# Performance work log

Measured on AMD Instinct MI355X. Metric: run time of the kernel, lower is better.

Reference implementation:

```python
import jax, jax.numpy as jnp
import numpy as np

B, L, D = 8, 4096, 768
EPS = 1e-5


def layer_norm(x, g, b):
    mu = jnp.mean(x, axis=-1, keepdims=True)
    var = jnp.mean(jnp.square(x - mu), axis=-1, keepdims=True)
    return (x - mu) * jax.lax.rsqrt(var + EPS) * g + b


def conv1d_same(x_blc, w_oik, b_o):
    # x_blc: [B, L, C] -> torch Conv1d(C, C, 3, padding=1) on [B, C, L]
    x_ncw = jnp.swapaxes(x_blc, 1, 2)
    y = jax.lax.conv_general_dilated(
        x_ncw, w_oik, window_strides=(1,), padding=[(1, 1)],
        dimension_numbers=("NCW", "OIW", "NCW"))
    y = y + b_o[None, :, None]
    return jnp.swapaxes(y, 1, 2)


def simple_ssm(u, a_p, b_p, c_p, d_p):
    # Diagonal SSM: h_t = sigmoid(a)*h_{t-1} + b*u_t ; y_t = c*h_t + d*u_t
    a = jax.nn.sigmoid(a_p)  # [D]

    def step(h, ut):  # h, ut: [B, D]
        h = a * h + b_p * ut
        return h, c_p * h

    h0 = jnp.zeros((u.shape[0], u.shape[2]), u.dtype)
    _, y = jax.lax.scan(step, h0, jnp.swapaxes(u, 0, 1))  # y: [L, B, D]
    return jnp.swapaxes(y, 0, 1) + d_p * u


def setup_inputs() -> dict:
    key = jax.random.key(0)
    ks = jax.random.split(key, 16)
    s_lin = 1.0 / np.sqrt(D)
    s_conv = 1.0 / np.sqrt(3 * D)
    return {
        "x": jax.random.normal(ks[0], (B, L, D), jnp.float32),
        "ln_g": jnp.ones((D,), jnp.float32),
        "ln_b": jnp.zeros((D,), jnp.float32),
        "Wi": jax.random.normal(ks[1], (D, 2 * D), jnp.float32) * s_lin,
        "bi": jnp.zeros((2 * D,), jnp.float32),
        "Wf_conv": jax.random.normal(ks[2], (D, D, 3), jnp.float32) * s_conv,
        "bf_conv": jnp.zeros((D,), jnp.float32),
        "af": jax.random.normal(ks[3], (D,), jnp.float32),
        "bf": jax.random.normal(ks[4], (D,), jnp.float32) * 0.5,
        "cf": jax.random.normal(ks[5], (D,), jnp.float32) * 0.5,
        "df": jax.random.normal(ks[6], (D,), jnp.float32) * 0.5,
        "Wb_conv": jax.random.normal(ks[7], (D, D, 3), jnp.float32) * s_conv,
        "bb_conv": jnp.zeros((D,), jnp.float32),
        "ab": jax.random.normal(ks[8], (D,), jnp.float32),
        "bb": jax.random.normal(ks[9], (D,), jnp.float32) * 0.5,
        "cb": jax.random.normal(ks[10], (D,), jnp.float32) * 0.5,
        "db": jax.random.normal(ks[11], (D,), jnp.float32) * 0.5,
        "Wo": jax.random.normal(ks[12], (D, D), jnp.float32) * s_lin,
        "bo": jnp.zeros((D,), jnp.float32),
    }


def reference(x, ln_g, ln_b, Wi, bi, Wf_conv, bf_conv, af, bf, cf, df,
              Wb_conv, bb_conv, ab, bb, cb, db, Wo, bo):
    residual = x
    xn = layer_norm(x, ln_g, ln_b)
    proj = xn @ Wi + bi                      # [B, L, 2D]
    xg, z = proj[..., :D], proj[..., D:]
    # forward branch
    f = conv1d_same(xg, Wf_conv, bf_conv)
    f = simple_ssm(f, af, bf, cf, df)
    # backward branch (flip along sequence)
    b_in = jnp.flip(xg, axis=1)
    bb_out = conv1d_same(b_in, Wb_conv, bb_conv)
    bb_out = simple_ssm(bb_out, ab, bb, cb, db)
    bb_out = jnp.flip(bb_out, axis=1)
    zg = jax.nn.silu(z)
    y = f * zg + bb_out * zg
    return y @ Wo + bo + residual
```

## Files before the change

kernel.cpp:

```cpp
#include <hip/hip_runtime.h>
#include <cstdint>
#include <cstddef>
#include <math.h>

#define L_SEQ 4096
#define D_DIM 768
#define B_SZ 8
#define M_ROWS (B_SZ * L_SEQ)
#define CHUNK 64

typedef __bf16 bf16x8 __attribute__((ext_vector_type(8)));
typedef float floatx4 __attribute__((ext_vector_type(4)));

#define GLP(p)  ((__attribute__((address_space(1))) const void*)(const void*)(p))
#define LDSP(p) ((__attribute__((address_space(3))) void*)(void*)(p))

__global__ __launch_bounds__(256) void ln_kernel(const float* __restrict__ x,
                                                 const float* __restrict__ g,
                                                 const float* __restrict__ b,
                                                 __bf16* __restrict__ xn) {
  __shared__ float red[256];
  const int tid = threadIdx.x;
  const size_t row = blockIdx.x;
  const float* xr = x + row * D_DIM;
  float v0 = xr[tid];
  float v1 = xr[tid + 256];
  float v2 = xr[tid + 512];
  red[tid] = v0 + v1 + v2;
  __syncthreads();
  for (int off = 128; off > 0; off >>= 1) {
    if (tid < off) red[tid] += red[tid + off];
    __syncthreads();
  }
  float mu = red[0] * (1.0f / D_DIM);
  __syncthreads();
  float d0 = v0 - mu, d1 = v1 - mu, d2 = v2 - mu;
  red[tid] = d0 * d0 + d1 * d1 + d2 * d2;
  __syncthreads();
  for (int off = 128; off > 0; off >>= 1) {
    if (tid < off) red[tid] += red[tid + off];
    __syncthreads();
  }
  float rs = rsqrtf(red[0] * (1.0f / D_DIM) + 1e-5f);
  __bf16* xo = xn + row * D_DIM;
  xo[tid]       = (__bf16)(d0 * rs * g[tid]       + b[tid]);
  xo[tid + 256] = (__bf16)(d1 * rs * g[tid + 256] + b[tid + 256]);
  xo[tid + 512] = (__bf16)(d2 * rs * g[tid + 512] + b[tid + 512]);
}


#define VMW(n) asm volatile("s_waitcnt vmcnt(" #n ")" ::: "memory")
#define BARR   asm volatile("s_barrier" ::: "memory")
#define MF(a, b, c) __builtin_amdgcn_mfma_f32_16x16x32_bf16((a), (b), (c), 0, 0, 0)
#define LDV(off) (*(const bf16x8*)(smem + (off)))

#define RDA(BUF, MOFF) do { \
  aR0k0 = LDV((BUF)*65536 + aoff + (MOFF) + ck0);        aR0k1 = LDV((BUF)*65536 + aoff + (MOFF) + ck1); \
  aR1k0 = LDV((BUF)*65536 + aoff + (MOFF) + 2048 + ck0); aR1k1 = LDV((BUF)*65536 + aoff + (MOFF) + 2048 + ck1); \
  aR2k0 = LDV((BUF)*65536 + aoff + (MOFF) + 4096 + ck0); aR2k1 = LDV((BUF)*65536 + aoff + (MOFF) + 4096 + ck1); \
  aR3k0 = LDV((BUF)*65536 + aoff + (MOFF) + 6144 + ck0); aR3k1 = LDV((BUF)*65536 + aoff + (MOFF) + 6144 + ck1); \
} while (0)

#define RDB01(BUF) do { \
  bN0k0 = LDV((BUF)*65536 + boff + ck0);        bN0k1 = LDV((BUF)*65536 + boff + ck1); \
  bN1k0 = LDV((BUF)*65536 + boff + 2048 + ck0); bN1k1 = LDV((BUF)*65536 + boff + 2048 + ck1); \
} while (0)

#define RDB23(BUF) do { \
  bN2k0 = LDV((BUF)*65536 + boff + 4096 + ck0); bN2k1 = LDV((BUF)*65536 + boff + 4096 + ck1); \
  bN3k0 = LDV((BUF)*65536 + boff + 6144 + ck0); bN3k1 = LDV((BUF)*65536 + boff + 6144 + ck1); \
} while (0)

#define MMQ01(AI) do { \
  acc[(AI)+0][0] = MF(aR0k0, bN0k0, acc[(AI)+0][0]); acc[(AI)+0][0] = MF(aR0k1, bN0k1, acc[(AI)+0][0]); \
  acc[(AI)+0][1] = MF(aR0k0, bN1k0, acc[(AI)+0][1]); acc[(AI)+0][1] = MF(aR0k1, bN1k1, acc[(AI)+0][1]); \
  acc[(AI)+1][0] = MF(aR1k0, bN0k0, acc[(AI)+1][0]); acc[(AI)+1][0] = MF(aR1k1, bN0k1, acc[(AI)+1][0]); \
  acc[(AI)+1][1] = MF(aR1k0, bN1k0, acc[(AI)+1][1]); acc[(AI)+1][1] = MF(aR1k1, bN1k1, acc[(AI)+1][1]); \
  acc[(AI)+2][0] = MF(aR2k0, bN0k0, acc[(AI)+2][0]); acc[(AI)+2][0] = MF(aR2k1, bN0k1, acc[(AI)+2][0]); \
  acc[(AI)+2][1] = MF(aR2k0, bN1k0, acc[(AI)+2][1]); acc[(AI)+2][1] = MF(aR2k1, bN1k1, acc[(AI)+2][1]); \
  acc[(AI)+3][0] = MF(aR3k0, bN0k0, acc[(AI)+3][0]); acc[(AI)+3][0] = MF(aR3k1, bN0k1, acc[(AI)+3][0]); \
  acc[(AI)+3][1] = MF(aR3k0, bN1k0, acc[(AI)+3][1]); acc[(AI)+3][1] = MF(aR3k1, bN1k1, acc[(AI)+3][1]); \
} while (0)

#define MMQ23(AI) do { \
  acc[(AI)+0][2] = MF(aR0k0, bN2k0, acc[(AI)+0][2]); acc[(AI)+0][2] = MF(aR0k1, bN2k1, acc[(AI)+0][2]); \
  acc[(AI)+0][3] = MF(aR0k0, bN3k0, acc[(AI)+0][3]); acc[(AI)+0][3] = MF(aR0k1, bN3k1, acc[(AI)+0][3]); \
  acc[(AI)+1][2] = MF(aR1k0, bN2k0, acc[(AI)+1][2]); acc[(AI)+1][2] = MF(aR1k1, bN2k1, acc[(AI)+1][2]); \
  acc[(AI)+1][3] = MF(aR1k0, bN3k0, acc[(AI)+1][3]); acc[(AI)+1][3] = MF(aR1k1, bN3k1, acc[(AI)+1][3]); \
  acc[(AI)+2][2] = MF(aR2k0, bN2k0, acc[(AI)+2][2]); acc[(AI)+2][2] = MF(aR2k1, bN2k1, acc[(AI)+2][2]); \
  acc[(AI)+2][3] = MF(aR2k0, bN3k0, acc[(AI)+2][3]); acc[(AI)+2][3] = MF(aR2k1, bN3k1, acc[(AI)+2][3]); \
  acc[(AI)+3][2] = MF(aR3k0, bN2k0, acc[(AI)+3][2]); acc[(AI)+3][2] = MF(aR3k1, bN2k1, acc[(AI)+3][2]); \
  acc[(AI)+3][3] = MF(aR3k0, bN3k0, acc[(AI)+3][3]); acc[(AI)+3][3] = MF(aR3k1, bN3k1, acc[(AI)+3][3]); \
} while (0)

#define STAGE_A_HP(h, p, tkt, BUF) do { \
  const __bf16* _s; \
  if (MODE == 1) { \
    const int _kb = ((tkt) * 43) >> 9;                        \
    const int _io = (((tkt) - _kb * 12) << 6) + (_kb - 1) * D_DIM; \
    _s = ((unsigned)(lv##h##p + _kb - 1) < (unsigned)L_SEQ) ? (rb##h##p + _io) : zbuf; \
  } else { \
    _s = rb##h##p + (tkt) * 64; \
  } \
  __builtin_amdgcn_global_load_lds(GLP(_s), \
      LDSP(smem + (BUF)*65536 + (h)*8192 + (p)*16384 + dstw), 16, 0, 0); \
} while (0)

#define STAGE_B_HP(h, p, tkt, BUF) \
  __builtin_amdgcn_global_load_lds(GLP(pB##h##p + (tkt) * 64), \
      LDSP(smem + (BUF)*65536 + 32768 + (h)*16384 + (p)*8192 + dstw), 16, 0, 0)

#define TILE(T, BUF, VA, VC, SA1, SREST) do { \
   \
  VMW(VA); BARR; \
  RDB01(BUF); RDA(BUF, 0); \
  if (SA1) { STAGE_A_HP(1, 0, (T) + 1, (BUF) ^ 1); STAGE_A_HP(1, 1, (T) + 1, (BUF) ^ 1); } \
  __builtin_amdgcn_s_setprio(1); MMQ01(0); __builtin_amdgcn_s_setprio(0); \
   \
  BARR; \
  RDB23(BUF); \
  if (SREST) { STAGE_A_HP(0, 0, (T) + 2, (BUF)); STAGE_A_HP(0, 1, (T) + 2, (BUF)); } \
  __builtin_amdgcn_s_setprio(1); MMQ23(0); __builtin_amdgcn_s_setprio(0); \
   \
  VMW(VC); BARR; \
  RDA(BUF, 8192); \
  if (SREST) { STAGE_B_HP(0, 0, (T) + 2, (BUF)); STAGE_B_HP(0, 1, (T) + 2, (BUF)); } \
  __builtin_amdgcn_s_setprio(1); MMQ01(4); __builtin_amdgcn_s_setprio(0); \
   \
  if (SREST) { STAGE_B_HP(1, 0, (T) + 2, (BUF)); STAGE_B_HP(1, 1, (T) + 2, (BUF)); } \
  __builtin_amdgcn_s_setprio(1); MMQ23(4); __builtin_amdgcn_s_setprio(0); \
} while (0)

template<int MODE, int NT, int NN>
__global__ __launch_bounds__(512) void gemm256_kernel(
    const __bf16* __restrict__ A, const __bf16* __restrict__ Bt,
    const float* __restrict__ bias_lo, const float* __restrict__ bias_hi,
    const float* __restrict__ resid,
    __bf16* __restrict__ out0, __bf16* __restrict__ out1,
    float* __restrict__ outf, const __bf16* __restrict__ zbuf) {
  extern __shared__ char smem[];
  constexpr int K = NT * 64;
  constexpr int nwg = NN * (M_ROWS / 256);
  constexpr int cpx = nwg / 8;
  const int bid = blockIdx.x;
  const int wgs = (bid & 7) * cpx + (bid >> 3);
  const int tileN = wgs % NN;
  const int tileM = wgs / NN;
  const int tid  = (int)threadIdx.x;
  const int w    = tid >> 6;
  const int lane = tid & 63;
  const int l15  = lane & 15;
  const int quad = lane >> 4;
  const int wm   = w >> 2;
  const int wn   = w & 3;

  const int srow = tid >> 3;
  const int ce   = ((tid & 7) ^ (srow & 7)) << 3;
  const int dstw = w << 10;

  const int aoff = (wm * 128 + l15) * 128;
  const int boff = 32768 + (wn * 64 + l15) * 128;
  const int ck0  = (quad ^ (l15 & 7)) << 4;
  const int ck1  = ((4 | quad) ^ (l15 & 7)) << 4;

  const __bf16* pB00 = Bt + (size_t)(tileN * 256 + srow) * K + ce;
  const __bf16* pB01 = Bt + (size_t)(tileN * 256 + 64 + srow) * K + ce;
  const __bf16* pB10 = Bt + (size_t)(tileN * 256 + 128 + srow) * K + ce;
  const __bf16* pB11 = Bt + (size_t)(tileN * 256 + 192 + srow) * K + ce;

  const __bf16 *rb00, *rb01, *rb10, *rb11;
  int lv00 = 0, lv01 = 0, lv10 = 0, lv11 = 0;
  {
    const int g00 = tileM * 256 + srow;
    const int g01 = tileM * 256 + 128 + srow;
    const int g10 = tileM * 256 + 64 + srow;
    const int g11 = tileM * 256 + 192 + srow;
    if (MODE == 1) {
      rb00 = A + (size_t)g00 * D_DIM + ce; lv00 = g00 & (L_SEQ - 1);
      rb01 = A + (size_t)g01 * D_DIM + ce; lv01 = g01 & (L_SEQ - 1);
      rb10 = A + (size_t)g10 * D_DIM + ce; lv10 = g10 & (L_SEQ - 1);
      rb11 = A + (size_t)g11 * D_DIM + ce; lv11 = g11 & (L_SEQ - 1);
    } else {
      rb00 = A + (size_t)g00 * K + ce;
      rb01 = A + (size_t)g01 * K + ce;
      rb10 = A + (size_t)g10 * K + ce;
      rb11 = A + (size_t)g11 * K + ce;
    }
  }

  bf16x8 aR0k0, aR0k1, aR1k0, aR1k1, aR2k0, aR2k1, aR3k0, aR3k1;
  bf16x8 bN0k0, bN0k1, bN1k0, bN1k1, bN2k0, bN2k1, bN3k0, bN3k1;
  floatx4 acc[8][4];
#pragma unroll
  for (int i = 0; i < 8; ++i)
#pragma unroll
    for (int j = 0; j < 4; ++j)
#pragma unroll
      for (int r = 0; r < 4; ++r) acc[i][j][r] = 0.0f;

  STAGE_A_HP(0, 0, 0, 0); STAGE_A_HP(0, 1, 0, 0);
  STAGE_B_HP(0, 0, 0, 0); STAGE_B_HP(0, 1, 0, 0);
  STAGE_B_HP(1, 0, 0, 0); STAGE_B_HP(1, 1, 0, 0);
  STAGE_A_HP(1, 0, 0, 0); STAGE_A_HP(1, 1, 0, 0);
  STAGE_A_HP(0, 0, 1, 1); STAGE_A_HP(0, 1, 1, 1);
  STAGE_B_HP(0, 0, 1, 1); STAGE_B_HP(0, 1, 1, 1);
  STAGE_B_HP(1, 0, 1, 1); STAGE_B_HP(1, 1, 1, 1);

  for (int it = 0; it < (NT - 2) / 2; ++it) {
    const int T0 = it * 2;
    TILE(T0,     0, 8, 10, 1, 1);
    TILE(T0 + 1, 1, 8, 10, 1, 1);
  }
  TILE(NT - 2, 0, 8, 8, 1, 0);
  TILE(NT - 1, 1, 2, 0, 0, 0);

  const int rowb = tileM * 256 + wm * 128 + quad * 4;
  const int colb = tileN * 256 + wn * 64 + l15;
#pragma unroll
  for (int mi = 0; mi < 8; ++mi) {
#pragma unroll
    for (int nj = 0; nj < 4; ++nj) {
      const int col = colb + nj * 16;
      float bv;
      if (MODE == 3) bv = bias_lo[col];
      else bv = (col < D_DIM) ? bias_lo[col] : bias_hi[col - D_DIM];
#pragma unroll
      for (int r = 0; r < 4; ++r) {
        const int row = rowb + mi * 16 + r;
        float v = acc[mi][nj][r] + bv;
        if (MODE == 3) {
          const size_t o = (size_t)row * D_DIM + col;
          outf[o] = v + resid[o];
        } else if (MODE == 0) {
          if (col < D_DIM) out0[(size_t)row * D_DIM + col] = (__bf16)v;
          else out1[(size_t)row * D_DIM + (col - D_DIM)] = (__bf16)(v / (1.0f + expf(-v)));
        } else {
          if (col < D_DIM) out0[(size_t)row * D_DIM + col] = (__bf16)v;
          else out1[(size_t)row * D_DIM + (col - D_DIM)] = (__bf16)v;
        }
      }
    }
  }
}

__global__ __launch_bounds__(256) void scan1_kernel(
    const float* __restrict__ ap0, const float* __restrict__ bp0,
    const float* __restrict__ ap1, const float* __restrict__ bp1,
    const __bf16* __restrict__ u0, const __bf16* __restrict__ u1,
    float* __restrict__ hl) {
  int idx = blockIdx.x * 256 + threadIdx.x;
  int dg = idx % 96;
  int rest = idx / 96;
  int chunk = rest & 63;
  int tb = rest >> 6;
  int tensor = tb >> 3;
  int b = tb & 7;
  const float* ap = (tensor ? ap1 : ap0) + dg * 8;
  const float* bp = (tensor ? bp1 : bp0) + dg * 8;
  const __bf16* u = (tensor ? u1 : u0) +
      ((size_t)(b * L_SEQ + chunk * CHUNK + (tensor ? CHUNK - 1 : 0))) * D_DIM + dg * 8;
  const int st = tensor ? -D_DIM : D_DIM;
  float a[8], bb[8], h[8];
#pragma unroll
  for (int j = 0; j < 8; ++j) {
    a[j] = 1.0f / (1.0f + expf(-ap[j]));
    bb[j] = bp[j];
    h[j] = 0.0f;
  }
  for (int t = 0; t < CHUNK; ++t) {
    bf16x8 uv = *(const bf16x8*)u;
#pragma unroll
    for (int j = 0; j < 8; ++j) h[j] = a[j] * h[j] + bb[j] * (float)uv[j];
    u += st;
  }
  float* o = hl + (size_t)(tb * 64 + chunk) * D_DIM + dg * 8;
#pragma unroll
  for (int j = 0; j < 8; ++j) o[j] = h[j];
}

__global__ __launch_bounds__(256) void scan2_kernel(
    const float* __restrict__ ap0, const float* __restrict__ ap1,
    float* __restrict__ hl) {
  int idx = blockIdx.x * 256 + threadIdx.x;
  int d = idx % D_DIM;
  int tb = idx / D_DIM;
  int tensor = tb >> 3;
  const float* ap = tensor ? ap1 : ap0;
  float a = 1.0f / (1.0f + expf(-ap[d]));
  float aT = a * a;  aT *= aT;  aT *= aT;  aT *= aT;  aT *= aT;  aT *= aT;
  float* p = hl + (size_t)tb * 64 * D_DIM + d + (tensor ? 63 * D_DIM : 0);
  const int st = tensor ? -D_DIM : D_DIM;
  float carry = 0.0f;
  for (int c = 0; c < 64; ++c) {
    float tmp = *p;
    *p = carry;
    carry = aT * carry + tmp;
    p += st;
  }
}

__global__ __launch_bounds__(256) void ssm_gate_kernel(
    const float* __restrict__ ap0, const float* __restrict__ bp0,
    const float* __restrict__ cp0, const float* __restrict__ dp0,
    const float* __restrict__ ap1, const float* __restrict__ bp1,
    const float* __restrict__ cp1, const float* __restrict__ dp1,
    __bf16* __restrict__ u0, const __bf16* __restrict__ u1,
    const __bf16* __restrict__ zg, __bf16* __restrict__ y,
    const float* __restrict__ hl) {
  int idx = blockIdx.x * 256 + threadIdx.x;
  int dg = idx % 96;
  int rest = idx / 96;
  int chunk = rest & 63;
  int b = rest >> 6;
  const size_t rowbase = (size_t)(b * L_SEQ + chunk * CHUNK) * D_DIM + dg * 8;

  {
    const float* ap = ap0 + dg * 8;
    const float* bp = bp0 + dg * 8;
    const float* cp = cp0 + dg * 8;
    const float* dp = dp0 + dg * 8;
    const float* hp = hl + (size_t)(b * 64 + chunk) * D_DIM + dg * 8;
    float a[8], bb[8], cc[8], dd[8], h[8];
#pragma unroll
    for (int j = 0; j < 8; ++j) {
      a[j] = 1.0f / (1.0f + expf(-ap[j]));
      bb[j] = bp[j]; cc[j] = cp[j]; dd[j] = dp[j];
      h[j] = hp[j];
    }
    __bf16* p = u0 + rowbase;
    for (int t = 0; t < CHUNK; ++t) {
      bf16x8 uv = *(const bf16x8*)p;
      bf16x8 ov;
#pragma unroll
      for (int j = 0; j < 8; ++j) {
        float xv = (float)uv[j];
        h[j] = a[j] * h[j] + bb[j] * xv;
        ov[j] = (__bf16)(cc[j] * h[j] + dd[j] * xv);
      }
      *(bf16x8*)p = ov;
      p += D_DIM;
    }
  }

  {
    const float* ap = ap1 + dg * 8;
    const float* bp = bp1 + dg * 8;
    const float* cp = cp1 + dg * 8;
    const float* dp = dp1 + dg * 8;
    const float* hp = hl + (size_t)((8 + b) * 64 + chunk) * D_DIM + dg * 8;
    float a[8], bb[8], cc[8], dd[8], h[8];
#pragma unroll
    for (int j = 0; j < 8; ++j) {
      a[j] = 1.0f / (1.0f + expf(-ap[j]));
      bb[j] = bp[j]; cc[j] = cp[j]; dd[j] = dp[j];
      h[j] = hp[j];
    }
    const size_t tail = rowbase + (size_t)(CHUNK - 1) * D_DIM;
    const __bf16* p1 = u1 + tail;
    const __bf16* pf = u0 + tail;
    const __bf16* pz = zg + tail;
    __bf16* py = y + tail;
    for (int t = 0; t < CHUNK; ++t) {
      bf16x8 uv = *(const bf16x8*)p1;
      bf16x8 f8 = *(const bf16x8*)pf;
      bf16x8 z8 = *(const bf16x8*)pz;
      bf16x8 ov;
#pragma unroll
      for (int j = 0; j < 8; ++j) {
        float xv = (float)uv[j];
        h[j] = a[j] * h[j] + bb[j] * xv;
        float bbv = cc[j] * h[j] + dd[j] * xv;
        ov[j] = (__bf16)(((float)f8[j] + bbv) * (float)z8[j]);
      }
      *(bf16x8*)py = ov;
      p1 -= D_DIM; pf -= D_DIM; pz -= D_DIM; py -= D_DIM;
    }
  }
}

__global__ __launch_bounds__(256) void tr32_kernel(const float* __restrict__ in,
                                                   __bf16* __restrict__ out,
                                                   int Kdim, int Ndim) {
  __shared__ float t[32][33];
  const int tx = threadIdx.x & 31;
  const int ty = threadIdx.x >> 5;
  const int n0 = blockIdx.x * 32;
  const int k0 = blockIdx.y * 32;
#pragma unroll
  for (int i = 0; i < 4; ++i)
    t[ty + i * 8][tx] = in[(size_t)(k0 + ty + i * 8) * Ndim + n0 + tx];
  __syncthreads();
#pragma unroll
  for (int i = 0; i < 4; ++i)
    out[(size_t)(n0 + ty + i * 8) * Kdim + k0 + tx] = (__bf16)t[tx][ty + i * 8];
}

__global__ __launch_bounds__(256) void trconv_kernel(const float* __restrict__ in,
                                                     __bf16* __restrict__ out,
                                                     int rev) {
  __shared__ float row[2304];
  const int o = blockIdx.x;
  const float* src = in + (size_t)o * 2304;
  for (int t = threadIdx.x; t < 2304; t += 256) row[t] = src[t];
  __syncthreads();
  __bf16* dst = out + (size_t)o * 2304;
  for (int t = threadIdx.x; t < 2304; t += 256) {
    int k = t / 768;
    int i = t - k * 768;
    int ks = rev ? (2 - k) : k;
    dst[t] = (__bf16)row[i * 3 + ks];
  }
}

__global__ void zero_kernel(__bf16* z) { z[threadIdx.x] = (__bf16)0.0f; }

extern "C" void kernel_launch(void* const* d_in, const int* in_sizes, int n_in,
                              void* d_out, int out_size, void* d_ws, size_t ws_size,
                              hipStream_t stream) {
  const float* x    = (const float*)d_in[0];
  const float* ln_g = (const float*)d_in[1];
  const float* ln_b = (const float*)d_in[2];
  const float* Wi   = (const float*)d_in[3];
  const float* bi   = (const float*)d_in[4];
  const float* Wf   = (const float*)d_in[5];
  const float* bfc  = (const float*)d_in[6];
  const float* af   = (const float*)d_in[7];
  const float* bfp  = (const float*)d_in[8];
  const float* cfp  = (const float*)d_in[9];
  const float* dfp  = (const float*)d_in[10];
  const float* Wb   = (const float*)d_in[11];
  const float* bbc  = (const float*)d_in[12];
  const float* ab   = (const float*)d_in[13];
  const float* bbp  = (const float*)d_in[14];
  const float* cbp  = (const float*)d_in[15];
  const float* dbp  = (const float*)d_in[16];
  const float* Wo   = (const float*)d_in[17];
  const float* bo   = (const float*)d_in[18];
  float* out = (float*)d_out;

  char* ws = (char*)d_ws;
  const size_t BLD = (size_t)B_SZ * L_SEQ * D_DIM;
  __bf16* ws0 = (__bf16*)(ws);
  __bf16* ws1 = (__bf16*)(ws + BLD * 2);
  __bf16* ws2 = (__bf16*)(ws + BLD * 4);
  __bf16* ws3 = (__bf16*)(ws + BLD * 6);
  __bf16* wit  = (__bf16*)(ws + BLD * 8);
  __bf16* wcat = wit + (size_t)1536 * 768;
  __bf16* wot  = wcat + (size_t)1536 * 2304;
  __bf16* zbuf = wot + (size_t)768 * 768;
  float* hl = (float*)wcat;
  const size_t needed = BLD * 8 +
      ((size_t)1536 * 768 + (size_t)1536 * 2304 + (size_t)768 * 768) * 2 + 256;
  if (ws_size < needed) return;

  static bool attr_done = false;
  if (!attr_done) {
    (void)hipFuncSetAttribute(reinterpret_cast<const void*>(&gemm256_kernel<0, 12, 6>),
                              hipFuncAttributeMaxDynamicSharedMemorySize, 131072);
    (void)hipFuncSetAttribute(reinterpret_cast<const void*>(&gemm256_kernel<1, 36, 6>),
                              hipFuncAttributeMaxDynamicSharedMemorySize, 131072);
    (void)hipFuncSetAttribute(reinterpret_cast<const void*>(&gemm256_kernel<3, 12, 3>),
                              hipFuncAttributeMaxDynamicSharedMemorySize, 131072);
    attr_done = true;
  }

  zero_kernel<<<1, 128, 0, stream>>>(zbuf);
  tr32_kernel<<<dim3(1536 / 32, 768 / 32), 256, 0, stream>>>(Wi, wit, 768, 1536);
  trconv_kernel<<<768, 256, 0, stream>>>(Wf, wcat, 0);
  trconv_kernel<<<768, 256, 0, stream>>>(Wb, wcat + (size_t)768 * 2304, 1);
  tr32_kernel<<<dim3(768 / 32, 768 / 32), 256, 0, stream>>>(Wo, wot, 768, 768);

  ln_kernel<<<M_ROWS, 256, 0, stream>>>(x, ln_g, ln_b, ws0);

  gemm256_kernel<0, 12, 6><<<768, 512, 131072, stream>>>(
      ws0, wit, bi, bi + 768, nullptr, ws1, ws2, nullptr, zbuf);

  gemm256_kernel<1, 36, 6><<<768, 512, 131072, stream>>>(
      ws1, wcat, bfc, bbc, nullptr, ws0, ws3, nullptr, zbuf);

  scan1_kernel<<<384, 256, 0, stream>>>(af, bfp, ab, bbp, ws0, ws3, hl);
  scan2_kernel<<<48, 256, 0, stream>>>(af, ab, hl);
  ssm_gate_kernel<<<192, 256, 0, stream>>>(af, bfp, cfp, dfp, ab, bbp, cbp, dbp,
                                           ws0, ws3, ws2, ws1, hl);

  gemm256_kernel<3, 12, 3><<<384, 512, 131072, stream>>>(
      ws1, wot, bo, bo, x, nullptr, nullptr, out, zbuf);
}
```

Before: 725.4 us.

## Prefetch next tile's LDS fragments into split A registers across GEMM phases

```diff
diff --git a/kernel.cpp b/kernel.cpp
--- a/kernel.cpp
+++ b/kernel.cpp
@@ -51,46 +51,77 @@
 
 #define VMW(n) asm volatile("s_waitcnt vmcnt(" #n ")" ::: "memory")
 #define BARR   asm volatile("s_barrier" ::: "memory")
+#define SP1    __builtin_amdgcn_s_setprio(1)
+#define SP0    __builtin_amdgcn_s_setprio(0)
 #define MF(a, b, c) __builtin_amdgcn_mfma_f32_16x16x32_bf16((a), (b), (c), 0, 0, 0)
 #define LDV(off) (*(const bf16x8*)(smem + (off)))
 
-#define RDA(BUF, MOFF) do { \
-  aR0k0 = LDV((BUF)*65536 + aoff + (MOFF) + ck0);        aR0k1 = LDV((BUF)*65536 + aoff + (MOFF) + ck1); \
-  aR1k0 = LDV((BUF)*65536 + aoff + (MOFF) + 2048 + ck0); aR1k1 = LDV((BUF)*65536 + aoff + (MOFF) + 2048 + ck1); \
-  aR2k0 = LDV((BUF)*65536 + aoff + (MOFF) + 4096 + ck0); aR2k1 = LDV((BUF)*65536 + aoff + (MOFF) + 4096 + ck1); \
-  aR3k0 = LDV((BUF)*65536 + aoff + (MOFF) + 6144 + ck0); aR3k1 = LDV((BUF)*65536 + aoff + (MOFF) + 6144 + ck1); \
-} while (0)
-
-#define RDB01(BUF) do { \
+#define RD_AL(BUF) do { \
+  aL0k0 = LDV((BUF)*65536 + aoff + ck0);        aL0k1 = LDV((BUF)*65536 + aoff + ck1); \
+  aL1k0 = LDV((BUF)*65536 + aoff + 2048 + ck0); aL1k1 = LDV((BUF)*65536 + aoff + 2048 + ck1); \
+  aL2k0 = LDV((BUF)*65536 + aoff + 4096 + ck0); aL2k1 = LDV((BUF)*65536 + aoff + 4096 + ck1); \
+  aL3k0 = LDV((BUF)*65536 + aoff + 6144 + ck0); aL3k1 = LDV((BUF)*65536 + aoff + 6144 + ck1); \
+} while (0)
+
+#define RD_AH(BUF) do { \
+  aH0k0 = LDV((BUF)*65536 + aoff + 8192 + ck0);        aH0k1 = LDV((BUF)*65536 + aoff + 8192 + ck1); \
+  aH1k0 = LDV((BUF)*65536 + aoff + 8192 + 2048 + ck0); aH1k1 = LDV((BUF)*65536 + aoff + 8192 + 2048 + ck1); \
+  aH2k0 = LDV((BUF)*65536 + aoff + 8192 + 4096 + ck0); aH2k1 = LDV((BUF)*65536 + aoff + 8192 + 4096 + ck1); \
+  aH3k0 = LDV((BUF)*65536 + aoff + 8192 + 6144 + ck0); aH3k1 = LDV((BUF)*65536 + aoff + 8192 + 6144 + ck1); \
+} while (0)
+
+#define RD_B01(BUF) do { \
   bN0k0 = LDV((BUF)*65536 + boff + ck0);        bN0k1 = LDV((BUF)*65536 + boff + ck1); \
   bN1k0 = LDV((BUF)*65536 + boff + 2048 + ck0); bN1k1 = LDV((BUF)*65536 + boff + 2048 + ck1); \
 } while (0)
 
-#define RDB23(BUF) do { \
+#define RD_B23(BUF) do { \
   bN2k0 = LDV((BUF)*65536 + boff + 4096 + ck0); bN2k1 = LDV((BUF)*65536 + boff + 4096 + ck1); \
   bN3k0 = LDV((BUF)*65536 + boff + 6144 + ck0); bN3k1 = LDV((BUF)*65536 + boff + 6144 + ck1); \
 } while (0)
 
-#define MMQ01(AI) do { \
-  acc[(AI)+0][0] = MF(aR0k0, bN0k0, acc[(AI)+0][0]); acc[(AI)+0][0] = MF(aR0k1, bN0k1, acc[(AI)+0][0]); \
-  acc[(AI)+0][1] = MF(aR0k0, bN1k0, acc[(AI)+0][1]); acc[(AI)+0][1] = MF(aR0k1, bN1k1, acc[(AI)+0][1]); \
-  acc[(AI)+1][0] = MF(aR1k0, bN0k0, acc[(AI)+1][0]); acc[(AI)+1][0] = MF(aR1k1, bN0k1, acc[(AI)+1][0]); \
-  acc[(AI)+1][1] = MF(aR1k0, bN1k0, acc[(AI)+1][1]); acc[(AI)+1][1] = MF(aR1k1, bN1k1, acc[(AI)+1][1]); \
-  acc[(AI)+2][0] = MF(aR2k0, bN0k0, acc[(AI)+2][0]); acc[(AI)+2][0] = MF(aR2k1, bN0k1, acc[(AI)+2][0]); \
-  acc[(AI)+2][1] = MF(aR2k0, bN1k0, acc[(AI)+2][1]); acc[(AI)+2][1] = MF(aR2k1, bN1k1, acc[(AI)+2][1]); \
-  acc[(AI)+3][0] = MF(aR3k0, bN0k0, acc[(AI)+3][0]); acc[(AI)+3][0] = MF(aR3k1, bN0k1, acc[(AI)+3][0]); \
-  acc[(AI)+3][1] = MF(aR3k0, bN1k0, acc[(AI)+3][1]); acc[(AI)+3][1] = MF(aR3k1, bN1k1, acc[(AI)+3][1]); \
-} while (0)
-
-#define MMQ23(AI) do { \
-  acc[(AI)+0][2] = MF(aR0k0, bN2k0, acc[(AI)+0][2]); acc[(AI)+0][2] = MF(aR0k1, bN2k1, acc[(AI)+0][2]); \
-  acc[(AI)+0][3] = MF(aR0k0, bN3k0, acc[(AI)+0][3]); acc[(AI)+0][3] = MF(aR0k1, bN3k1, acc[(AI)+0][3]); \
-  acc[(AI)+1][2] = MF(aR1k0, bN2k0, acc[(AI)+1][2]); acc[(AI)+1][2] = MF(aR1k1, bN2k1, acc[(AI)+1][2]); \
-  acc[(AI)+1][3] = MF(aR1k0, bN3k0, acc[(AI)+1][3]); acc[(AI)+1][3] = MF(aR1k1, bN3k1, acc[(AI)+1][3]); \
-  acc[(AI)+2][2] = MF(aR2k0, bN2k0, acc[(AI)+2][2]); acc[(AI)+2][2] = MF(aR2k1, bN2k1, acc[(AI)+2][2]); \
-  acc[(AI)+2][3] = MF(aR2k0, bN3k0, acc[(AI)+2][3]); acc[(AI)+2][3] = MF(aR2k1, bN3k1, acc[(AI)+2][3]); \
-  acc[(AI)+3][2] = MF(aR3k0, bN2k0, acc[(AI)+3][2]); acc[(AI)+3][2] = MF(aR3k1, bN2k1, acc[(AI)+3][2]); \
-  acc[(AI)+3][3] = MF(aR3k0, bN3k0, acc[(AI)+3][3]); acc[(AI)+3][3] = MF(aR3k1, bN3k1, acc[(AI)+3][3]); \
+#define MMQ01L do { \
+  acc[0][0] = MF(aL0k0, bN0k0, acc[0][0]); acc[0][0] = MF(aL0k1, bN0k1, acc[0][0]); \
+  acc[0][1] = MF(aL0k0, bN1k0, acc[0][1]); acc[0][1] = MF(aL0k1, bN1k1, acc[0][1]); \
+  acc[1][0] = MF(aL1k0, bN0k0, acc[1][0]); acc[1][0] = MF(aL1k1, bN0k1, acc[1][0]); \
+  acc[1][1] = MF(aL1k0, bN1k0, acc[1][1]); acc[1][1] = MF(aL1k1, bN1k1, acc[1][1]); \
+  acc[2][0] = MF(aL2k0, bN0k0, acc[2][0]); acc[2][0] = MF(aL2k1, bN0k1, acc[2][0]); \
+  acc[2][1] = MF(aL2k0, bN1k0, acc[2][1]); acc[2][1] = MF(aL2k1, bN1k1, acc[2][1]); \
+  acc[3][0] = MF(aL3k0, bN0k0, acc[3][0]); acc[3][0] = MF(aL3k1, bN0k1, acc[3][0]); \
+  acc[3][1] = MF(aL3k0, bN1k0, acc[3][1]); acc[3][1] = MF(aL3k1, bN1k1, acc[3][1]); \
+} while (0)
+
+#define MMQ23L do { \
+  acc[0][2] = MF(aL0k0, bN2k0, acc[0][2]); acc[0][2] = MF(aL0k1, bN2k1, acc[0][2]); \
+  acc[0][3] = MF(aL0k0, bN3k0, acc[0][3]); acc[0][3] = MF(aL0k1, bN3k1, acc[0][3]); \
+  acc[1][2] = MF(aL1k0, bN2k0, acc[1][2]); acc[1][2] = MF(aL1k1, bN2k1, acc[1][2]); \
+  acc[1][3] = MF(aL1k0, bN3k0, acc[1][3]); acc[1][3] = MF(aL1k1, bN3k1, acc[1][3]); \
+  acc[2][2] = MF(aL2k0, bN2k0, acc[2][2]); acc[2][2] = MF(aL2k1, bN2k1, acc[2][2]); \
+  acc[2][3] = MF(aL2k0, bN3k0, acc[2][3]); acc[2][3] = MF(aL2k1, bN3k1, acc[2][3]); \
+  acc[3][2] = MF(aL3k0, bN2k0, acc[3][2]); acc[3][2] = MF(aL3k1, bN2k1, acc[3][2]); \
+  acc[3][3] = MF(aL3k0, bN3k0, acc[3][3]); acc[3][3] = MF(aL3k1, bN3k1, acc[3][3]); \
+} while (0)
+
+#define MMQ01H do { \
+  acc[4][0] = MF(aH0k0, bN0k0, acc[4][0]); acc[4][0] = MF(aH0k1, bN0k1, acc[4][0]); \
+  acc[4][1] = MF(aH0k0, bN1k0, acc[4][1]); acc[4][1] = MF(aH0k1, bN1k1, acc[4][1]); \
+  acc[5][0] = MF(aH1k0, bN0k0, acc[5][0]); acc[5][0] = MF(aH1k1, bN0k1, acc[5][0]); \
+  acc[5][1] = MF(aH1k0, bN1k0, acc[5][1]); acc[5][1] = MF(aH1k1, bN1k1, acc[5][1]); \
+  acc[6][0] = MF(aH2k0, bN0k0, acc[6][0]); acc[6][0] = MF(aH2k1, bN0k1, acc[6][0]); \
+  acc[6][1] = MF(aH2k0, bN1k0, acc[6][1]); acc[6][1] = MF(aH2k1, bN1k1, acc[6][1]); \
+  acc[7][0] = MF(aH3k0, bN0k0, acc[7][0]); acc[7][0] = MF(aH3k1, bN0k1, acc[7][0]); \
+  acc[7][1] = MF(aH3k0, bN1k0, acc[7][1]); acc[7][1] = MF(aH3k1, bN1k1, acc[7][1]); \
+} while (0)
+
+#define MMQ23H do { \
+  acc[4][2] = MF(aH0k0, bN2k0, acc[4][2]); acc[4][2] = MF(aH0k1, bN2k1, acc[4][2]); \
+  acc[4][3] = MF(aH0k0, bN3k0, acc[4][3]); acc[4][3] = MF(aH0k1, bN3k1, acc[4][3]); \
+  acc[5][2] = MF(aH1k0, bN2k0, acc[5][2]); acc[5][2] = MF(aH1k1, bN2k1, acc[5][2]); \
+  acc[5][3] = MF(aH1k0, bN3k0, acc[5][3]); acc[5][3] = MF(aH1k1, bN3k1, acc[5][3]); \
+  acc[6][2] = MF(aH2k0, bN2k0, acc[6][2]); acc[6][2] = MF(aH2k1, bN2k1, acc[6][2]); \
+  acc[6][3] = MF(aH2k0, bN3k0, acc[6][3]); acc[6][3] = MF(aH2k1, bN3k1, acc[6][3]); \
+  acc[7][2] = MF(aH3k0, bN2k0, acc[7][2]); acc[7][2] = MF(aH3k1, bN2k1, acc[7][2]); \
+  acc[7][3] = MF(aH3k0, bN3k0, acc[7][3]); acc[7][3] = MF(aH3k1, bN3k1, acc[7][3]); \
 } while (0)
 
 #define STAGE_A_HP(h, p, tkt, BUF) do { \
@@ -110,25 +141,26 @@
   __builtin_amdgcn_global_load_lds(GLP(pB##h##p + (tkt) * 64), \
       LDSP(smem + (BUF)*65536 + 32768 + (h)*16384 + (p)*8192 + dstw), 16, 0, 0)
 
-#define TILE(T, BUF, VA, VC, SA1, SREST) do { \
+#define TILE(T, BUF, VA, VC, SA1, SREST, DORD) do { \
    \
   VMW(VA); BARR; \
-  RDB01(BUF); RDA(BUF, 0); \
+  RD_B23(BUF); \
   if (SA1) { STAGE_A_HP(1, 0, (T) + 1, (BUF) ^ 1); STAGE_A_HP(1, 1, (T) + 1, (BUF) ^ 1); } \
-  __builtin_amdgcn_s_setprio(1); MMQ01(0); __builtin_amdgcn_s_setprio(0); \
+  SP1; MMQ01L; SP0; \
    \
   BARR; \
-  RDB23(BUF); \
+  RD_AH(BUF); \
   if (SREST) { STAGE_A_HP(0, 0, (T) + 2, (BUF)); STAGE_A_HP(0, 1, (T) + 2, (BUF)); } \
-  __builtin_amdgcn_s_setprio(1); MMQ23(0); __builtin_amdgcn_s_setprio(0); \
+  SP1; MMQ23L; SP0; \
    \
   VMW(VC); BARR; \
-  RDA(BUF, 8192); \
+  if (DORD) { RD_AL((BUF) ^ 1); } \
   if (SREST) { STAGE_B_HP(0, 0, (T) + 2, (BUF)); STAGE_B_HP(0, 1, (T) + 2, (BUF)); } \
-  __builtin_amdgcn_s_setprio(1); MMQ01(4); __builtin_amdgcn_s_setprio(0); \
+  SP1; MMQ01H; SP0; \
    \
+  if (DORD) { RD_B01((BUF) ^ 1); } \
   if (SREST) { STAGE_B_HP(1, 0, (T) + 2, (BUF)); STAGE_B_HP(1, 1, (T) + 2, (BUF)); } \
-  __builtin_amdgcn_s_setprio(1); MMQ23(4); __builtin_amdgcn_s_setprio(0); \
+  SP1; MMQ23H; SP0; \
 } while (0)
 
 template<int MODE, int NT, int NN>
@@ -188,7 +220,8 @@
     }
   }
 
-  bf16x8 aR0k0, aR0k1, aR1k0, aR1k1, aR2k0, aR2k1, aR3k0, aR3k1;
+  bf16x8 aL0k0, aL0k1, aL1k0, aL1k1, aL2k0, aL2k1, aL3k0, aL3k1;
+  bf16x8 aH0k0, aH0k1, aH1k0, aH1k1, aH2k0, aH2k1, aH3k0, aH3k1;
   bf16x8 bN0k0, bN0k1, bN1k0, bN1k1, bN2k0, bN2k1, bN3k0, bN3k1;
   floatx4 acc[8][4];
 #pragma unroll
@@ -205,14 +238,17 @@
   STAGE_A_HP(0, 0, 1, 1); STAGE_A_HP(0, 1, 1, 1);
   STAGE_B_HP(0, 0, 1, 1); STAGE_B_HP(0, 1, 1, 1);
   STAGE_B_HP(1, 0, 1, 1); STAGE_B_HP(1, 1, 1, 1);
+  VMW(6);
+  BARR;
+  RD_AL(0); RD_B01(0);
 
   for (int it = 0; it < (NT - 2) / 2; ++it) {
     const int T0 = it * 2;
-    TILE(T0,     0, 8, 10, 1, 1);
-    TILE(T0 + 1, 1, 8, 10, 1, 1);
-  }
-  TILE(NT - 2, 0, 8, 8, 1, 0);
-  TILE(NT - 1, 1, 2, 0, 0, 0);
+    TILE(T0,     0, 6, 6, 1, 1, 1);
+    TILE(T0 + 1, 1, 6, 6, 1, 1, 1);
+  }
+  TILE(NT - 2, 0, 6, 4, 1, 0, 1);
+  TILE(NT - 1, 1, 0, 63, 0, 0, 0);
 
   const int rowb = tileM * 256 + wm * 128 + quad * 4;
   const int colb = tileN * 256 + wn * 64 + l15;
```

Result: slower. 1.224 ms (+68.7%).
